# Performance work log

Measured on AMD Instinct MI355X. Metric: run time of the kernel, lower is better.

Reference implementation:

```python
import jax, jax.numpy as jnp
import numpy as np

N_NODES = 100000
N_EDGES = 1600000
D_IN, D_HID, D_OUT = 128, 64, 40


def glorot(key, shape):
    lim = float(np.sqrt(6.0 / (shape[0] + shape[1])))
    return jax.random.uniform(key, shape, jnp.float32, -lim, lim)


def gcn_layer(x, W, b, src, dst, d_inv):
    # PyG GCNConv: linear first, then sym-normalized aggregation with self-loops.
    h = x @ W  # [N, d_out]
    coef = (d_inv[src] * d_inv[dst])[:, None]       # [E, 1]
    msg = h[src] * coef                              # [E, d_out] gather
    agg = jax.ops.segment_sum(msg, dst, num_segments=N_NODES)  # scatter-add
    agg = agg + h * (d_inv * d_inv)[:, None]         # self-loop contribution
    return agg + b


def setup_inputs() -> dict:
    key = jax.random.key(0)
    ks = jax.random.split(key, 8)
    x = jax.random.normal(ks[0], (N_NODES, D_IN), jnp.float32)
    edge_index = jax.random.randint(ks[1], (2, N_EDGES), 0, N_NODES, jnp.int64)
    return {
        "x": x,
        "edge_index": edge_index,
        "W1": glorot(ks[2], (D_IN, D_HID)), "b1": jnp.zeros((D_HID,), jnp.float32),
        "W2": glorot(ks[3], (D_HID, D_HID)), "b2": jnp.zeros((D_HID,), jnp.float32),
        "W3": glorot(ks[4], (D_HID, D_OUT)), "b3": jnp.zeros((D_OUT,), jnp.float32),
    }


def reference(x, edge_index, W1, b1, W2, b2, W3, b3):
    src, dst = edge_index[0], edge_index[1]
    # degree with self-loops (each node gets +1)
    deg = jax.ops.segment_sum(jnp.ones((N_EDGES,), jnp.float32), dst,
                              num_segments=N_NODES) + 1.0
    d_inv = jax.lax.rsqrt(deg)
    h = jax.nn.relu(gcn_layer(x, W1, b1, src, dst, d_inv))
    h = jax.nn.relu(gcn_layer(h, W2, b2, src, dst, d_inv))
    return gcn_layer(h, W3, b3, src, dst, d_inv)
```

## Files before the change

### kernel.cpp

```cpp
#include <hip/hip_runtime.h>
#include <hip/hip_bf16.h>


constexpr int BLK = 256;
constexpr int SB2 = 9;
constexpr int EPB = 4096;
constexpr int BUCKCAP = 10240;

typedef __attribute__((ext_vector_type(8))) short bf16x8;
typedef __attribute__((ext_vector_type(4))) float f32x4;

__device__ inline unsigned short bf_rne(float f) {
    unsigned int u = __float_as_uint(f);
    unsigned int r = (u + 0x7fffu + ((u >> 16) & 1u)) >> 16;
    return (unsigned short)r;
}
__device__ inline unsigned int pk(unsigned short lo, unsigned short hi) {
    return (unsigned int)lo | ((unsigned int)hi << 16);
}

__global__ __launch_bounds__(256) void part_hist(
    const int* __restrict__ dst, int* __restrict__ bh, int E, int nblk, int NB2) {
    __shared__ int lh[256];
    int k = blockIdx.x, t = threadIdx.x;
    lh[t] = 0;
    __syncthreads();
    const int4* dp = (const int4*)(dst + k * EPB);
#pragma unroll
    for (int j = 0; j < EPB / 1024; ++j) {
        int idx = j * 256 + t;
        int e = k * EPB + idx * 4;
        if (e < E) {
            int4 d4 = dp[idx];
            atomicAdd(&lh[d4.x >> SB2], 1);
            atomicAdd(&lh[d4.y >> SB2], 1);
            atomicAdd(&lh[d4.z >> SB2], 1);
            atomicAdd(&lh[d4.w >> SB2], 1);
        }
    }
    __syncthreads();
    if (t < NB2) bh[t * nblk + k] = lh[t];
}

__global__ __launch_bounds__(256) void part_scan(
    int* __restrict__ bh, int* __restrict__ btot, int nblk) {
    __shared__ int sh[256];
    int b = blockIdx.x, t = threadIdx.x;
    int base = b * BUCKCAP;
    int v[4]; int s = 0;
#pragma unroll
    for (int j = 0; j < 4; ++j) {
        int idx = t * 4 + j;
        v[j] = (idx < nblk) ? bh[b * nblk + idx] : 0;
        s += v[j];
    }
    sh[t] = s;
    __syncthreads();
    for (int off = 1; off < 256; off <<= 1) {
        int x = (t >= off) ? sh[t - off] : 0;
        __syncthreads();
        sh[t] += x;
        __syncthreads();
    }
    int run = sh[t] - s;
    if (t == 255) btot[b] = (sh[255] < BUCKCAP) ? sh[255] : BUCKCAP;
#pragma unroll
    for (int j = 0; j < 4; ++j) {
        int idx = t * 4 + j;
        if (idx < nblk) bh[b * nblk + idx] = base + run;
        run += v[j];
    }
}

__global__ __launch_bounds__(256) void part_scatter(
    const int* __restrict__ src, const int* __restrict__ dst,
    const int* __restrict__ bh, unsigned int* __restrict__ buf,
    int E, int nblk, int NB2) {
    __shared__ int lbase[256];
    __shared__ int lcnt[256];
    int k = blockIdx.x, t = threadIdx.x;
    lcnt[t] = 0;
    if (t < NB2) lbase[t] = bh[t * nblk + k];
    __syncthreads();
    const int4* dp = (const int4*)(dst + k * EPB);
    const int4* sp = (const int4*)(src + k * EPB);
#pragma unroll
    for (int j = 0; j < EPB / 1024; ++j) {
        int idx = j * 256 + t;
        int e = k * EPB + idx * 4;
        if (e < E) {
            int4 d4 = dp[idx];
            int4 s4 = sp[idx];
            int d, bkt, p;
            d = d4.x; bkt = d >> SB2; p = lbase[bkt] + atomicAdd(&lcnt[bkt], 1);
            buf[p] = ((unsigned int)(d & 511) << 23) | (unsigned int)s4.x;
            d = d4.y; bkt = d >> SB2; p = lbase[bkt] + atomicAdd(&lcnt[bkt], 1);
            buf[p] = ((unsigned int)(d & 511) << 23) | (unsigned int)s4.y;
            d = d4.z; bkt = d >> SB2; p = lbase[bkt] + atomicAdd(&lcnt[bkt], 1);
            buf[p] = ((unsigned int)(d & 511) << 23) | (unsigned int)s4.z;
            d = d4.w; bkt = d >> SB2; p = lbase[bkt] + atomicAdd(&lcnt[bkt], 1);
            buf[p] = ((unsigned int)(d & 511) << 23) | (unsigned int)s4.w;
        }
    }
}

__global__ __launch_bounds__(256) void csr_finalize(
    const unsigned int* __restrict__ buf, const int* __restrict__ btot,
    int* __restrict__ rptr, int* __restrict__ rdeg, float* __restrict__ dinv,
    int* __restrict__ csr, int N) {
    __shared__ int hist[1 << SB2];
    __shared__ int excl[1 << SB2];
    __shared__ int ssc[256];
    int b = blockIdx.x, t = threadIdx.x;
    int nb0 = b << SB2;
    int nn = N - nb0; if (nn > (1 << SB2)) nn = 1 << SB2;
    int beg = b * BUCKCAP;
    int end = beg + btot[b];

    hist[t] = 0; hist[t + 256] = 0;
    __syncthreads();
    for (int i = beg + t; i < end; i += 256)
        atomicAdd(&hist[buf[i] >> 23], 1);
    __syncthreads();

    int a0 = hist[2 * t], a1 = hist[2 * t + 1];
    int s = a0 + a1;
    ssc[t] = s;
    __syncthreads();
    for (int off = 1; off < 256; off <<= 1) {
        int x = (t >= off) ? ssc[t - off] : 0;
        __syncthreads();
        ssc[t] += x;
        __syncthreads();
    }
    int run = ssc[t] - s;
    excl[2 * t] = run;
    excl[2 * t + 1] = run + a0;
    __syncthreads();

    for (int j = t; j < nn; j += 256) {
        rptr[nb0 + j] = beg + excl[j];
        rdeg[nb0 + j] = hist[j];
        dinv[nb0 + j] = rsqrtf((float)hist[j] + 1.0f);
    }
    __syncthreads();

    hist[t] = 0; hist[t + 256] = 0;
    __syncthreads();
    for (int i = beg + t; i < end; i += 256) {
        unsigned int w = buf[i];
        int local = w >> 23;
        int p = beg + excl[local] + atomicAdd(&hist[local], 1);
        csr[p] = (int)(w & 0x7fffffu);
    }
}

template<int K, int NOUT, int HSTRIDE, bool AFP32>
__global__ __launch_bounds__(256) void gemm_mfma(
    const void* __restrict__ Aptr, const float* __restrict__ W,
    const float* __restrict__ d_inv, unsigned short* __restrict__ hs, int M)
{
    __shared__ unsigned short Wt[64][K + 8];
    __shared__ float Cst[64][68];

    const int t = threadIdx.x;
    const int wave = t >> 6, lane = t & 63;
    const int m = lane & 15, kq = lane >> 4;

    for (int idx = t; idx < K * 64; idx += 256) {
        int k = idx >> 6, c = idx & 63;
        float wv = (c < NOUT) ? W[k * NOUT + c] : 0.0f;
        Wt[c][k] = bf_rne(wv);
    }
    __syncthreads();

    const int rb = blockIdx.x * 64;
    int arow = rb + wave * 16 + m;
    if (arow >= M) arow = M - 1;

    f32x4 acc[4] = {{0.f,0.f,0.f,0.f},{0.f,0.f,0.f,0.f},
                    {0.f,0.f,0.f,0.f},{0.f,0.f,0.f,0.f}};
    union Frag { bf16x8 v; unsigned short u[8]; };

#pragma unroll
    for (int kc = 0; kc < K / 32; ++kc) {
        const int kbase = kc * 32 + kq * 8;
        Frag a;
        if (AFP32) {
            const float* ap = (const float*)Aptr + (size_t)arow * K + kbase;
            float4 x0 = *(const float4*)ap;
            float4 x1 = *(const float4*)(ap + 4);
            a.u[0] = bf_rne(x0.x); a.u[1] = bf_rne(x0.y);
            a.u[2] = bf_rne(x0.z); a.u[3] = bf_rne(x0.w);
            a.u[4] = bf_rne(x1.x); a.u[5] = bf_rne(x1.y);
            a.u[6] = bf_rne(x1.z); a.u[7] = bf_rne(x1.w);
        } else {
            const unsigned short* ap = (const unsigned short*)Aptr + (size_t)arow * 64 + kbase;
            a.v = *(const bf16x8*)ap;
        }
#pragma unroll
        for (int ct = 0; ct < 4; ++ct) {
            Frag b;
            b.v = *(const bf16x8*)(&Wt[ct * 16 + m][kbase]);
            acc[ct] = __builtin_amdgcn_mfma_f32_16x16x32_bf16(a.v, b.v, acc[ct], 0, 0, 0);
        }
    }

#pragma unroll
    for (int ct = 0; ct < 4; ++ct)
#pragma unroll
        for (int r = 0; r < 4; ++r)
            Cst[wave * 16 + kq * 4 + r][ct * 16 + m] = acc[ct][r];
    __syncthreads();

    int row = t >> 2, seg = t & 3;
    int grow = rb + row;
    int c0 = seg * 16;
    if (grow < M && c0 < NOUT) {
        float di = d_inv[grow];
        unsigned int uu[8];
#pragma unroll
        for (int j = 0; j < 8; ++j) {
            float v0 = Cst[row][c0 + 2 * j]     * di;
            float v1 = Cst[row][c0 + 2 * j + 1] * di;
            uu[j] = pk(bf_rne(v0), bf_rne(v1));
        }
        unsigned short* orow = hs + (size_t)grow * HSTRIDE + c0;
        *(uint4*)orow = make_uint4(uu[0], uu[1], uu[2], uu[3]);
        if (NOUT - c0 > 8)
            *((uint4*)orow + 1) = make_uint4(uu[4], uu[5], uu[6], uu[7]);
    }
}

template<int DACT, int HSTRIDE, bool RELU, bool OBF16, int OSTRIDE>
__global__ __launch_bounds__(256) void agg4(
    const unsigned short* __restrict__ hs, const int* __restrict__ rptr,
    const int* __restrict__ rdeg, const int* __restrict__ csr,
    const float* __restrict__ dinv, const float* __restrict__ b,
    void* __restrict__ out, int N)
{
    int i = (blockIdx.x * 256 + threadIdx.x) >> 4;
    if (i >= N) return;
    int lane = threadIdx.x & 63;
    int q  = lane & 15;
    int sb = lane & 48;
    constexpr int QACT = DACT / 4;
    const bool act = (q < QACT);

    int beg = rptr[i];
    int end = beg + rdeg[i];

    float a0 = 0.f, a1 = 0.f, a2 = 0.f, a3 = 0.f;
    if (act) {
        uint2 u0 = *(const uint2*)(hs + (size_t)i * HSTRIDE + q * 4);
        a0 = __uint_as_float(u0.x << 16);
        a1 = __uint_as_float(u0.x & 0xffff0000u);
        a2 = __uint_as_float(u0.y << 16);
        a3 = __uint_as_float(u0.y & 0xffff0000u);
    }

    for (int c = beg; c < end; c += 16) {
        int s_l = (c + q < end) ? csr[c + q] : 0;
        int m = end - c; if (m > 16) m = 16;
        int k = 0;
        for (; k + 8 <= m; k += 8) {
            int ss[8];
#pragma unroll
            for (int j = 0; j < 8; ++j) ss[j] = __shfl(s_l, sb | (k + j), 64);
            if (act) {
                uint2 vv[8];
#pragma unroll
                for (int j = 0; j < 8; ++j)
                    vv[j] = *(const uint2*)(hs + (size_t)ss[j] * HSTRIDE + q * 4);
#pragma unroll
                for (int j = 0; j < 8; ++j) {
                    a0 += __uint_as_float(vv[j].x << 16);
                    a1 += __uint_as_float(vv[j].x & 0xffff0000u);
                    a2 += __uint_as_float(vv[j].y << 16);
                    a3 += __uint_as_float(vv[j].y & 0xffff0000u);
                }
            }
        }
        for (; k < m; ++k) {
            int s = __shfl(s_l, sb | k, 64);
            if (act) {
                uint2 u = *(const uint2*)(hs + (size_t)s * HSTRIDE + q * 4);
                a0 += __uint_as_float(u.x << 16);
                a1 += __uint_as_float(u.x & 0xffff0000u);
                a2 += __uint_as_float(u.y << 16);
                a3 += __uint_as_float(u.y & 0xffff0000u);
            }
        }
    }

    if (act) {
        float di = dinv[i];
        const float4 bv = *(const float4*)(b + q * 4);
        a0 = di * a0 + bv.x; a1 = di * a1 + bv.y;
        a2 = di * a2 + bv.z; a3 = di * a3 + bv.w;
        if (RELU) {
            a0 = fmaxf(a0, 0.f); a1 = fmaxf(a1, 0.f);
            a2 = fmaxf(a2, 0.f); a3 = fmaxf(a3, 0.f);
        }
        if (OBF16) {
            unsigned short* ob = (unsigned short*)out;
            uint2 o;
            o.x = pk(bf_rne(a0), bf_rne(a1));
            o.y = pk(bf_rne(a2), bf_rne(a3));
            *(uint2*)(ob + (size_t)i * 64 + q * 4) = o;
        } else {
            float* of = (float*)out;
            *(float4*)(of + (size_t)i * OSTRIDE + q * 4) = make_float4(a0, a1, a2, a3);
        }
    }
}

extern "C" void kernel_launch(void* const* d_in, const int* in_sizes, int n_in,
                              void* d_out, int out_size, void* d_ws, size_t ws_size,
                              hipStream_t stream) {
    const float* x   = (const float*)d_in[0];
    const int*   ei  = (const int*)  d_in[1];
    const float* W1  = (const float*)d_in[2];
    const float* bb1 = (const float*)d_in[3];
    const float* W2  = (const float*)d_in[4];
    const float* bb2 = (const float*)d_in[5];
    const float* W3  = (const float*)d_in[6];
    const float* bb3 = (const float*)d_in[7];
    float* out = (float*)d_out;

    const int N = in_sizes[0] / 128;
    const int E = in_sizes[1] / 2;
    const int* src = ei;
    const int* dst = ei + E;
    const int NB2  = (N + (1 << SB2) - 1) >> SB2;
    const int nblk = (E + EPB - 1) / EPB;

    float* ws = (float*)d_ws;
    const size_t NP  = ((size_t)N + 255) & ~255ull;
    float* dinv = ws;
    unsigned short* bufHs  = (unsigned short*)(ws + NP);
    unsigned short* bufAct = bufHs + (size_t)N * 64;
    int*   rptr  = (int*)(bufAct + (size_t)N * 64);
    int*   rdeg  = rptr + N;
    int*   btot  = rdeg + N;
    int*   bh    = btot + 256;
    size_t bhsz  = ((size_t)NB2 * nblk + 1) & ~1ull;
    unsigned int* buf = (unsigned int*)(bh + bhsz);
    int*   csr   = (int*)(buf + (size_t)NB2 * BUCKCAP);

    dim3 blk(BLK);
    int gRows = (N + 63) / 64;
    int gQW   = (N * 16 + BLK - 1) / BLK;

    part_hist<<<nblk, blk, 0, stream>>>(dst, bh, E, nblk, NB2);
    part_scan<<<NB2, blk, 0, stream>>>(bh, btot, nblk);
    part_scatter<<<nblk, blk, 0, stream>>>(src, dst, bh, buf, E, nblk, NB2);
    csr_finalize<<<NB2, blk, 0, stream>>>(buf, btot, rptr, rdeg, dinv, csr, N);

    gemm_mfma<128, 64, 64, true><<<gRows, blk, 0, stream>>>(x, W1, dinv, bufHs, N);
    agg4<64, 64, true, true, 64><<<gQW, blk, 0, stream>>>(bufHs, rptr, rdeg, csr, dinv, bb1, bufAct, N);

    gemm_mfma<64, 64, 64, false><<<gRows, blk, 0, stream>>>(bufAct, W2, dinv, bufHs, N);
    agg4<64, 64, true, true, 64><<<gQW, blk, 0, stream>>>(bufHs, rptr, rdeg, csr, dinv, bb2, bufAct, N);

    gemm_mfma<64, 40, 40, false><<<gRows, blk, 0, stream>>>(bufAct, W3, dinv, bufHs, N);
    agg4<40, 40, false, false, 40><<<gQW, blk, 0, stream>>>(bufHs, rptr, rdeg, csr, dinv, bb3, out, N);
}
```

Baseline: 286.9 us.

## Fuse CSR-build kernels into one persistent kernel with grid barriers

Merges the four partitioning kernels (histogram, scan, scatter, finalize) into one kernel that uses atomic-counter grid barriers between phases, which requires a memset of the barrier counter. The goal is to remove three kernel launch gaps and their tail effects. With nblk of about 391 blocks, all blocks must be co-resident or the spin barrier deadlocks; launch_bounds(256,2) is meant to help with that. The aggregation kernel also hoists the dinv and bias loads ahead of the neighbour loop so their latency overlaps with the gathers.

```diff
diff --git a/kernel.cpp b/kernel.cpp
--- a/kernel.cpp
+++ b/kernel.cpp
@@ -19,139 +19,149 @@
     return (unsigned int)lo | ((unsigned int)hi << 16);
 }
 
-__global__ __launch_bounds__(256) void part_hist(
-    const int* __restrict__ dst, int* __restrict__ bh, int E, int nblk, int NB2) {
-    __shared__ int lh[256];
-    int k = blockIdx.x, t = threadIdx.x;
-    lh[t] = 0;
-    __syncthreads();
-    const int4* dp = (const int4*)(dst + k * EPB);
-#pragma unroll
-    for (int j = 0; j < EPB / 1024; ++j) {
-        int idx = j * 256 + t;
-        int e = k * EPB + idx * 4;
-        if (e < E) {
-            int4 d4 = dp[idx];
-            atomicAdd(&lh[d4.x >> SB2], 1);
-            atomicAdd(&lh[d4.y >> SB2], 1);
-            atomicAdd(&lh[d4.z >> SB2], 1);
-            atomicAdd(&lh[d4.w >> SB2], 1);
-        }
-    }
-    __syncthreads();
-    if (t < NB2) bh[t * nblk + k] = lh[t];
-}
-
-__global__ __launch_bounds__(256) void part_scan(
-    int* __restrict__ bh, int* __restrict__ btot, int nblk) {
-    __shared__ int sh[256];
-    int b = blockIdx.x, t = threadIdx.x;
-    int base = b * BUCKCAP;
-    int v[4]; int s = 0;
-#pragma unroll
-    for (int j = 0; j < 4; ++j) {
-        int idx = t * 4 + j;
-        v[j] = (idx < nblk) ? bh[b * nblk + idx] : 0;
-        s += v[j];
-    }
-    sh[t] = s;
-    __syncthreads();
-    for (int off = 1; off < 256; off <<= 1) {
-        int x = (t >= off) ? sh[t - off] : 0;
-        __syncthreads();
-        sh[t] += x;
-        __syncthreads();
-    }
-    int run = sh[t] - s;
-    if (t == 255) btot[b] = (sh[255] < BUCKCAP) ? sh[255] : BUCKCAP;
-#pragma unroll
-    for (int j = 0; j < 4; ++j) {
-        int idx = t * 4 + j;
-        if (idx < nblk) bh[b * nblk + idx] = base + run;
-        run += v[j];
-    }
-}
-
-__global__ __launch_bounds__(256) void part_scatter(
+__device__ inline void gridbar(int* bar, int target) {
+    __threadfence();
+    __syncthreads();
+    if (threadIdx.x == 0) {
+        __hip_atomic_fetch_add(bar, 1, __ATOMIC_ACQ_REL, __HIP_MEMORY_SCOPE_AGENT);
+        while (__hip_atomic_load(bar, __ATOMIC_RELAXED, __HIP_MEMORY_SCOPE_AGENT) < target)
+            __builtin_amdgcn_s_sleep(1);
+    }
+    __syncthreads();
+    __threadfence();
+}
+
+__global__ __launch_bounds__(256, 2) void partition_all(
     const int* __restrict__ src, const int* __restrict__ dst,
-    const int* __restrict__ bh, unsigned int* __restrict__ buf,
-    int E, int nblk, int NB2) {
-    __shared__ int lbase[256];
-    __shared__ int lcnt[256];
-    int k = blockIdx.x, t = threadIdx.x;
-    lcnt[t] = 0;
-    if (t < NB2) lbase[t] = bh[t * nblk + k];
-    __syncthreads();
-    const int4* dp = (const int4*)(dst + k * EPB);
-    const int4* sp = (const int4*)(src + k * EPB);
-#pragma unroll
-    for (int j = 0; j < EPB / 1024; ++j) {
-        int idx = j * 256 + t;
-        int e = k * EPB + idx * 4;
-        if (e < E) {
-            int4 d4 = dp[idx];
-            int4 s4 = sp[idx];
-            int d, bkt, p;
-            d = d4.x; bkt = d >> SB2; p = lbase[bkt] + atomicAdd(&lcnt[bkt], 1);
-            buf[p] = ((unsigned int)(d & 511) << 23) | (unsigned int)s4.x;
-            d = d4.y; bkt = d >> SB2; p = lbase[bkt] + atomicAdd(&lcnt[bkt], 1);
-            buf[p] = ((unsigned int)(d & 511) << 23) | (unsigned int)s4.y;
-            d = d4.z; bkt = d >> SB2; p = lbase[bkt] + atomicAdd(&lcnt[bkt], 1);
-            buf[p] = ((unsigned int)(d & 511) << 23) | (unsigned int)s4.z;
-            d = d4.w; bkt = d >> SB2; p = lbase[bkt] + atomicAdd(&lcnt[bkt], 1);
-            buf[p] = ((unsigned int)(d & 511) << 23) | (unsigned int)s4.w;
-        }
-    }
-}
-
-__global__ __launch_bounds__(256) void csr_finalize(
-    const unsigned int* __restrict__ buf, const int* __restrict__ btot,
+    int* __restrict__ bh, int* __restrict__ btot,
+    unsigned int* __restrict__ buf,
     int* __restrict__ rptr, int* __restrict__ rdeg, float* __restrict__ dinv,
-    int* __restrict__ csr, int N) {
-    __shared__ int hist[1 << SB2];
-    __shared__ int excl[1 << SB2];
-    __shared__ int ssc[256];
-    int b = blockIdx.x, t = threadIdx.x;
-    int nb0 = b << SB2;
-    int nn = N - nb0; if (nn > (1 << SB2)) nn = 1 << SB2;
-    int beg = b * BUCKCAP;
-    int end = beg + btot[b];
-
-    hist[t] = 0; hist[t + 256] = 0;
-    __syncthreads();
-    for (int i = beg + t; i < end; i += 256)
-        atomicAdd(&hist[buf[i] >> 23], 1);
-    __syncthreads();
-
-    int a0 = hist[2 * t], a1 = hist[2 * t + 1];
-    int s = a0 + a1;
-    ssc[t] = s;
-    __syncthreads();
-    for (int off = 1; off < 256; off <<= 1) {
-        int x = (t >= off) ? ssc[t - off] : 0;
-        __syncthreads();
-        ssc[t] += x;
-        __syncthreads();
-    }
-    int run = ssc[t] - s;
-    excl[2 * t] = run;
-    excl[2 * t + 1] = run + a0;
-    __syncthreads();
-
-    for (int j = t; j < nn; j += 256) {
-        rptr[nb0 + j] = beg + excl[j];
-        rdeg[nb0 + j] = hist[j];
-        dinv[nb0 + j] = rsqrtf((float)hist[j] + 1.0f);
-    }
-    __syncthreads();
-
-    hist[t] = 0; hist[t + 256] = 0;
-    __syncthreads();
-    for (int i = beg + t; i < end; i += 256) {
-        unsigned int w = buf[i];
-        int local = w >> 23;
-        int p = beg + excl[local] + atomicAdd(&hist[local], 1);
-        csr[p] = (int)(w & 0x7fffffu);
+    int* __restrict__ csr, int* __restrict__ bar,
+    int E, int nblk, int NB2, int N)
+{
+    __shared__ int smA[512];
+    __shared__ int smB[512];
+    __shared__ int smC[256];
+    const int k = blockIdx.x, t = threadIdx.x;
+
+    smA[t] = 0;
+    __syncthreads();
+    {
+        const int4* dp = (const int4*)(dst + k * EPB);
+#pragma unroll
+        for (int j = 0; j < EPB / 1024; ++j) {
+            int idx = j * 256 + t;
+            int e = k * EPB + idx * 4;
+            if (e < E) {
+                int4 d4 = dp[idx];
+                atomicAdd(&smA[d4.x >> SB2], 1);
+                atomicAdd(&smA[d4.y >> SB2], 1);
+                atomicAdd(&smA[d4.z >> SB2], 1);
+                atomicAdd(&smA[d4.w >> SB2], 1);
+            }
+        }
+    }
+    __syncthreads();
+    if (t < NB2) bh[t * nblk + k] = smA[t];
+
+    gridbar(bar, nblk);
+
+    if (k < NB2) {
+        int base = k * BUCKCAP;
+        int i0 = t * 4;
+        int v0 = (i0     < nblk) ? bh[k * nblk + i0    ] : 0;
+        int v1 = (i0 + 1 < nblk) ? bh[k * nblk + i0 + 1] : 0;
+        int v2 = (i0 + 2 < nblk) ? bh[k * nblk + i0 + 2] : 0;
+        int v3 = (i0 + 3 < nblk) ? bh[k * nblk + i0 + 3] : 0;
+        int s = v0 + v1 + v2 + v3;
+        smC[t] = s;
+        __syncthreads();
+        for (int off = 1; off < 256; off <<= 1) {
+            int x = (t >= off) ? smC[t - off] : 0;
+            __syncthreads();
+            smC[t] += x;
+            __syncthreads();
+        }
+        int run = smC[t] - s;
+        if (t == 255) btot[k] = (smC[255] < BUCKCAP) ? smC[255] : BUCKCAP;
+        if (i0     < nblk) bh[k * nblk + i0    ] = base + run; run += v0;
+        if (i0 + 1 < nblk) bh[k * nblk + i0 + 1] = base + run; run += v1;
+        if (i0 + 2 < nblk) bh[k * nblk + i0 + 2] = base + run; run += v2;
+        if (i0 + 3 < nblk) bh[k * nblk + i0 + 3] = base + run;
+    }
+
+    gridbar(bar, 2 * nblk);
+
+    smB[t] = 0;
+    if (t < NB2) smA[t] = bh[t * nblk + k];
+    __syncthreads();
+    {
+        const int4* dp = (const int4*)(dst + k * EPB);
+        const int4* sp = (const int4*)(src + k * EPB);
+#pragma unroll
+        for (int j = 0; j < EPB / 1024; ++j) {
+            int idx = j * 256 + t;
+            int e = k * EPB + idx * 4;
+            if (e < E) {
+                int4 d4 = dp[idx];
+                int4 s4 = sp[idx];
+                int d, bkt, p;
+                d = d4.x; bkt = d >> SB2; p = smA[bkt] + atomicAdd(&smB[bkt], 1);
+                buf[p] = ((unsigned int)(d & 511) << 23) | (unsigned int)s4.x;
+                d = d4.y; bkt = d >> SB2; p = smA[bkt] + atomicAdd(&smB[bkt], 1);
+                buf[p] = ((unsigned int)(d & 511) << 23) | (unsigned int)s4.y;
+                d = d4.z; bkt = d >> SB2; p = smA[bkt] + atomicAdd(&smB[bkt], 1);
+                buf[p] = ((unsigned int)(d & 511) << 23) | (unsigned int)s4.z;
+                d = d4.w; bkt = d >> SB2; p = smA[bkt] + atomicAdd(&smB[bkt], 1);
+                buf[p] = ((unsigned int)(d & 511) << 23) | (unsigned int)s4.w;
+            }
+        }
+    }
+
+    gridbar(bar, 3 * nblk);
+
+    if (k < NB2) {
+        int nb0 = k << SB2;
+        int nn = N - nb0; if (nn > (1 << SB2)) nn = 1 << SB2;
+        int beg = k * BUCKCAP;
+        int end = beg + btot[k];
+
+        smA[t] = 0; smA[t + 256] = 0;
+        __syncthreads();
+        for (int i = beg + t; i < end; i += 256)
+            atomicAdd(&smA[buf[i] >> 23], 1);
+        __syncthreads();
+
+        int a0 = smA[2 * t], a1 = smA[2 * t + 1];
+        int s = a0 + a1;
+        smC[t] = s;
+        __syncthreads();
+        for (int off = 1; off < 256; off <<= 1) {
+            int x = (t >= off) ? smC[t - off] : 0;
+            __syncthreads();
+            smC[t] += x;
+            __syncthreads();
+        }
+        int run = smC[t] - s;
+        smB[2 * t] = run;
+        smB[2 * t + 1] = run + a0;
+        __syncthreads();
+
+        for (int j = t; j < nn; j += 256) {
+            rptr[nb0 + j] = beg + smB[j];
+            rdeg[nb0 + j] = smA[j];
+            dinv[nb0 + j] = rsqrtf((float)smA[j] + 1.0f);
+        }
+        __syncthreads();
+
+        smA[t] = 0; smA[t + 256] = 0;
+        __syncthreads();
+        for (int i = beg + t; i < end; i += 256) {
+            unsigned int w = buf[i];
+            int local = w >> 23;
+            int p = beg + smB[local] + atomicAdd(&smA[local], 1);
+            csr[p] = (int)(w & 0x7fffffu);
+        }
     }
 }
 
@@ -251,7 +261,11 @@
     int end = beg + rdeg[i];
 
     float a0 = 0.f, a1 = 0.f, a2 = 0.f, a3 = 0.f;
+    float di = 0.f;
+    float4 bv = make_float4(0.f, 0.f, 0.f, 0.f);
     if (act) {
+        di = dinv[i];
+        bv = *(const float4*)(b + q * 4);
         uint2 u0 = *(const uint2*)(hs + (size_t)i * HSTRIDE + q * 4);
         a0 = __uint_as_float(u0.x << 16);
         a1 = __uint_as_float(u0.x & 0xffff0000u);
@@ -294,8 +308,6 @@
     }
 
     if (act) {
-        float di = dinv[i];
-        const float4 bv = *(const float4*)(b + q * 4);
         a0 = di * a0 + bv.x; a1 = di * a1 + bv.y;
         a2 = di * a2 + bv.z; a3 = di * a3 + bv.w;
         if (RELU) {
@@ -347,15 +359,16 @@
     size_t bhsz  = ((size_t)NB2 * nblk + 1) & ~1ull;
     unsigned int* buf = (unsigned int*)(bh + bhsz);
     int*   csr   = (int*)(buf + (size_t)NB2 * BUCKCAP);
+    int*   bar   = csr + (size_t)NB2 * BUCKCAP;
 
     dim3 blk(BLK);
     int gRows = (N + 63) / 64;
     int gQW   = (N * 16 + BLK - 1) / BLK;
 
-    part_hist<<<nblk, blk, 0, stream>>>(dst, bh, E, nblk, NB2);
-    part_scan<<<NB2, blk, 0, stream>>>(bh, btot, nblk);
-    part_scatter<<<nblk, blk, 0, stream>>>(src, dst, bh, buf, E, nblk, NB2);
-    csr_finalize<<<NB2, blk, 0, stream>>>(buf, btot, rptr, rdeg, dinv, csr, N);
+    hipMemsetAsync(bar, 0, 16, stream);
+    partition_all<<<nblk, blk, 0, stream>>>(src, dst, bh, btot, buf,
+                                            rptr, rdeg, dinv, csr, bar,
+                                            E, nblk, NB2, N);
 
     gemm_mfma<128, 64, 64, true><<<gRows, blk, 0, stream>>>(x, W1, dinv, bufHs, N);
     agg4<64, 64, true, true, 64><<<gQW, blk, 0, stream>>>(bufHs, rptr, rdeg, csr, dinv, bb1, bufAct, N);
```

Result: slower. 568.1 us (+98.0%).
